# Kernel optimization log

Hardware: AMD Instinct MI355X
Metric: run time of the kernel (lower is better)

Reference implementation:

```python
import jax, jax.numpy as jnp
import numpy as np

N, E = 50000, 800000
IN_F, OUT_F, H = 128, 128, 4
D = OUT_F // H  # head dim
NEG_SLOPE = 0.2
EPS = 1e-12


def setup_inputs() -> dict:
    key = jax.random.key(0)
    ks = jax.random.split(key, 10)
    s = 1.0 / np.sqrt(IN_F)
    return {
        "x": jax.random.normal(ks[0], (N, IN_F), jnp.float32),
        "W_src": jax.random.normal(ks[1], (IN_F, H * D), jnp.float32) * s,
        "b_src": jnp.zeros((H * D,), jnp.float32),
        "W_dst": jax.random.normal(ks[2], (IN_F, H * D), jnp.float32) * s,
        "b_dst": jnp.zeros((H * D,), jnp.float32),
        "attn": jax.random.normal(ks[3], (H, D), jnp.float32) * (1.0 / np.sqrt(D)),
        "out_bias": jnp.zeros((H * D,), jnp.float32),
        "ln_w": jnp.ones((OUT_F,), jnp.float32),
        "ln_b": jnp.zeros((OUT_F,), jnp.float32),
        "src": jax.random.randint(ks[4], (E,), 0, N, jnp.int32),
        "dst": jax.random.randint(ks[5], (E,), 0, N, jnp.int32),
    }


def reference(x, W_src, b_src, W_dst, b_dst, attn, out_bias, ln_w, ln_b, src, dst):
    n = x.shape[0]
    # GATv2Conv (share_weights=False): separate source/dest projections
    fs = (x @ W_src + b_src).reshape(n, H, D)  # [N,H,D]
    fd = (x @ W_dst + b_dst).reshape(n, H, D)
    # per-edge scores: e_ij = attn . leaky_relu(fs[u] + fd[v])
    e = jax.nn.leaky_relu(fs[src] + fd[dst], NEG_SLOPE)  # [E,H,D]
    logits = jnp.einsum("ehd,hd->eh", e, attn)  # [E,H]
    # edge softmax over incoming edges of each dst node
    m = jax.ops.segment_max(logits, dst, num_segments=n)  # [N,H]
    ex = jnp.exp(logits - m[dst])
    denom = jax.ops.segment_sum(ex, dst, num_segments=n)  # [N,H]
    alpha = ex / denom[dst]  # [E,H]
    # aggregate: sum_j alpha_ij * fs[j]
    msg = alpha[:, :, None] * fs[src]  # [E,H,D]
    rst = jax.ops.segment_sum(msg, dst, num_segments=n)  # [N,H,D]
    h = rst.reshape(n, H * D) + out_bias
    # LayerNorm (biased variance, eps inside sqrt)
    u = h.mean(-1, keepdims=True)
    s = jnp.mean((h - u) ** 2, -1, keepdims=True)
    h = (h - u) / jnp.sqrt(s + EPS)
    h = ln_w * h + ln_b
    # activation = elu; dropout p=0 -> identity
    return jax.nn.elu(h)
```

## Files before the change

### kernel.cpp

```cpp
#include <hip/hip_runtime.h>
#include <hip/hip_bf16.h>

constexpr int NF = 128;

using bf16x8 = __attribute__((ext_vector_type(8))) short;
using f32x4v = __attribute__((ext_vector_type(4))) float;

__device__ __forceinline__ unsigned short f2bs(float f) {
    return __builtin_bit_cast(unsigned short, __float2bfloat16(f));
}
__device__ __forceinline__ void unpack8(float4 raw, float* a) {
    unsigned u0 = __float_as_uint(raw.x);
    unsigned u1 = __float_as_uint(raw.y);
    unsigned u2 = __float_as_uint(raw.z);
    unsigned u3 = __float_as_uint(raw.w);
    a[0] = __uint_as_float(u0 << 16);
    a[1] = __uint_as_float(u0 & 0xffff0000u);
    a[2] = __uint_as_float(u1 << 16);
    a[3] = __uint_as_float(u1 & 0xffff0000u);
    a[4] = __uint_as_float(u2 << 16);
    a[5] = __uint_as_float(u2 & 0xffff0000u);
    a[6] = __uint_as_float(u3 << 16);
    a[7] = __uint_as_float(u3 & 0xffff0000u);
}

__global__ void GraphAttnLayer_70196945486348_kernel() {}

__global__ __launch_bounds__(256) void prep_kernel(
    const float* __restrict__ Wsrc, const float* __restrict__ Wdst,
    unsigned short* __restrict__ Wb,
    int* __restrict__ cnt, int* __restrict__ state, int N, int NB)
{
    int i = blockIdx.x * 256 + threadIdx.x;
    if (i < N) cnt[i] = 0;
    if (i < NB) state[i] = 0;
    if (i < 256 * NF) {
        int k   = i >> 8;
        int col = i & 255;
        float v = (col < 128) ? Wsrc[k * NF + col] : Wdst[k * NF + (col - 128)];
        Wb[col * NF + k] = f2bs(v);
    }
}

__global__ __launch_bounds__(256) void gemm_hist_kernel(
    const float* __restrict__ x,
    const unsigned short* __restrict__ Wb,
    const float* __restrict__ bsrc, const float* __restrict__ bdst,
    unsigned short* __restrict__ fs,
    float* __restrict__ fd,
    const int* __restrict__ src, const int* __restrict__ dst,
    int* __restrict__ cnt, int* __restrict__ pack,
    int N, int E, int NGB)
{
    {
        int e = blockIdx.x * 256 + threadIdx.x;
        if (e < E) {
            int r = atomicAdd(&cnt[dst[e]], 1);
            pack[e] = (r << 17) | src[e];
        }
    }
    if (blockIdx.x >= NGB) return;

    const int lane = threadIdx.x & 63;
    const int wave = threadIdx.x >> 6;
    const int m_base = blockIdx.x * 32;
    const int lm = lane & 15;
    const int kq = (lane >> 4) * 8;

    bf16x8 bfrag[4][4];
    float bias[4];
#pragma unroll
    for (int c = 0; c < 4; ++c) {
        int col = wave * 64 + c * 16 + lm;
        bias[c] = (col < 128) ? bsrc[col] : bdst[col - 128];
#pragma unroll
        for (int s = 0; s < 4; ++s)
            bfrag[c][s] = *(const bf16x8*)(Wb + col * NF + s * 32 + kq);
    }

    for (int r = 0; r < 2; ++r) {
        int m0 = m_base + r * 16;
        if (m0 >= N) break;
        int row = m0 + lm;
        if (row >= N) row = N - 1;
        bf16x8 afrag[4];
#pragma unroll
        for (int s = 0; s < 4; ++s) {
            const float4* xp = (const float4*)(x + (size_t)row * NF + s * 32 + kq);
            float4 xa = xp[0], xb = xp[1];
            afrag[s][0] = (short)f2bs(xa.x);
            afrag[s][1] = (short)f2bs(xa.y);
            afrag[s][2] = (short)f2bs(xa.z);
            afrag[s][3] = (short)f2bs(xa.w);
            afrag[s][4] = (short)f2bs(xb.x);
            afrag[s][5] = (short)f2bs(xb.y);
            afrag[s][6] = (short)f2bs(xb.z);
            afrag[s][7] = (short)f2bs(xb.w);
        }
#pragma unroll
        for (int c = 0; c < 4; ++c) {
            f32x4v acc = {0.f, 0.f, 0.f, 0.f};
#pragma unroll
            for (int s = 0; s < 4; ++s)
                acc = __builtin_amdgcn_mfma_f32_16x16x32_bf16(afrag[s], bfrag[c][s], acc, 0, 0, 0);
            int col = wave * 64 + c * 16 + lm;
            int cc = col & 127;
#pragma unroll
            for (int rr = 0; rr < 4; ++rr) {
                int rowd = m0 + (lane >> 4) * 4 + rr;
                if (rowd < N) {
                    float v = acc[rr] + bias[c];
                    if (col < 128) fs[(size_t)rowd * NF + cc] = f2bs(v);
                    else           fd[(size_t)rowd * NF + cc] = v;
                }
            }
        }
    }
}

__global__ __launch_bounds__(256) void scan_kernel(
    const int* __restrict__ cnt, int* __restrict__ rowptr,
    int* __restrict__ state, int N, int E)
{
    int b = blockIdx.x, t = threadIdx.x;
    int i = b * 256 + t;
    int v = (i < N) ? cnt[i] : 0;

    __shared__ int arr[256];
    __shared__ int s_bofs;
    arr[t] = v;
    __syncthreads();
    for (int off = 1; off < 256; off <<= 1) {
        int u = (t >= off) ? arr[t - off] : 0;
        __syncthreads();
        arr[t] += u;
        __syncthreads();
    }
    int total = arr[255];

    if (t < 64) {
        if (t == 0) {
            int word = ((b == 0 ? 2 : 1) << 30) | total;
            atomicExch(&state[b], word);
        }
        int bofs = 0;
        if (b > 0) {
            int base = b;
            for (;;) {
                int j = base - 1 - t;
                int sv = 0, f = 1;
                if (j >= 0) {
                    sv = atomicAdd(&state[j], 0);
                    f = ((unsigned)sv) >> 30;
                }
                unsigned long long notready = __ballot(f == 0);
                if (notready) continue;
                unsigned long long has2 = __ballot(f == 2);
                if (has2) {
                    int k = (int)(__ffsll((unsigned long long)has2) - 1);
                    int val = (t <= k) ? (sv & 0x3FFFFFFF) : 0;
#pragma unroll
                    for (int off = 32; off; off >>= 1) val += __shfl_xor(val, off);
                    bofs += val;
                    break;
                } else {
                    int val = (j >= 0) ? (sv & 0x3FFFFFFF) : 0;
#pragma unroll
                    for (int off = 32; off; off >>= 1) val += __shfl_xor(val, off);
                    bofs += val;
                    base -= 64;
                }
            }
            if (t == 0) atomicExch(&state[b], (2 << 30) | (bofs + total));
        }
        if (t == 0) s_bofs = bofs;
    }
    __syncthreads();
    int bofs = s_bofs;
    int excl = arr[t] - v + bofs;
    if (i < N) rowptr[i] = excl;
    if (i == 0) rowptr[N] = E;
}

__global__ __launch_bounds__(256) void scatter_kernel(
    const int* __restrict__ dst, const int* __restrict__ pack,
    const int* __restrict__ rowptr, int* __restrict__ src_sorted, int E)
{
    int idx = blockIdx.x * 256 + threadIdx.x;
    int e0 = idx * 4;
    if (e0 + 3 < E) {
        int4 d = *(const int4*)(dst + e0);
        int4 p = *(const int4*)(pack + e0);
        src_sorted[rowptr[d.x] + (p.x >> 17)] = p.x & 0x1FFFF;
        src_sorted[rowptr[d.y] + (p.y >> 17)] = p.y & 0x1FFFF;
        src_sorted[rowptr[d.z] + (p.z >> 17)] = p.z & 0x1FFFF;
        src_sorted[rowptr[d.w] + (p.w >> 17)] = p.w & 0x1FFFF;
    } else {
        for (int e = e0; e < E; ++e) {
            int p = pack[e];
            src_sorted[rowptr[dst[e]] + (p >> 17)] = p & 0x1FFFF;
        }
    }
}

__global__ __launch_bounds__(256) void node_kernel(
    const float4* __restrict__ fsq,
    const int* __restrict__ rowptr, const int* __restrict__ src_sorted,
    const float4* __restrict__ attn4,
    const float4* __restrict__ obias4,
    const float4* __restrict__ lnw4,
    const float4* __restrict__ lnb4,
    float4* __restrict__ out4, int N)
{
    int lane = threadIdx.x & 63;
    int es = lane >> 4;
    int g  = lane & 15;
    int n = blockIdx.x * 4 + (threadIdx.x >> 6);
    if (n >= N) return;

    float4 fda = out4[(size_t)n * 32 + g * 2];
    float4 fdb = out4[(size_t)n * 32 + g * 2 + 1];
    float4 ava = attn4[g * 2];
    float4 avb = attn4[g * 2 + 1];
    float fd[8] = {fda.x, fda.y, fda.z, fda.w, fdb.x, fdb.y, fdb.z, fdb.w};
    float av[8] = {ava.x, ava.y, ava.z, ava.w, avb.x, avb.y, avb.z, avb.w};

    int beg = rowptr[n], end = rowptr[n + 1];
    float l = 0.f;
    float ac[8] = {0.f, 0.f, 0.f, 0.f, 0.f, 0.f, 0.f, 0.f};

    for (int j = beg; j < end; j += 4) {
        int idx = j + es;
        bool valid = idx < end;
        int s = src_sorted[valid ? idx : (end - 1)];
        float4 raw = fsq[(size_t)s * 16 + g];
        float a[8];
        unpack8(raw, a);
        float p = 0.f;
#pragma unroll
        for (int d = 0; d < 8; ++d) {
            float t = a[d] + fd[d];
            t = fmaxf(t, 0.2f * t);
            p += av[d] * t;
        }
        p += __shfl_xor(p, 1);
        p += __shfl_xor(p, 2);
        float e = valid ? __expf(p) : 0.f;
        l += e;
#pragma unroll
        for (int d = 0; d < 8; ++d) ac[d] += e * a[d];
    }

    l += __shfl_xor(l, 16);
    l += __shfl_xor(l, 32);
#pragma unroll
    for (int d = 0; d < 8; ++d) {
        ac[d] += __shfl_xor(ac[d], 16);
        ac[d] += __shfl_xor(ac[d], 32);
    }

    float rl = (l > 0.f) ? (1.f / l) : 0.f;
    float4 oba = obias4[g * 2];
    float4 obb = obias4[g * 2 + 1];
    float ob[8] = {oba.x, oba.y, oba.z, oba.w, obb.x, obb.y, obb.z, obb.w};
    float h[8];
    float s1 = 0.f, s2 = 0.f;
#pragma unroll
    for (int d = 0; d < 8; ++d) {
        h[d] = ac[d] * rl + ob[d];
        s1 += h[d];
        s2 += h[d] * h[d];
    }
    s1 += __shfl_xor(s1, 1); s2 += __shfl_xor(s2, 1);
    s1 += __shfl_xor(s1, 2); s2 += __shfl_xor(s2, 2);
    s1 += __shfl_xor(s1, 4); s2 += __shfl_xor(s2, 4);
    s1 += __shfl_xor(s1, 8); s2 += __shfl_xor(s2, 8);

    float u = s1 * (1.f / NF);
    float var = s2 * (1.f / NF) - u * u;
    float rstd = rsqrtf(fmaxf(var, 0.f) + 1e-12f);
    float4 gwa = lnw4[g * 2], gwb = lnw4[g * 2 + 1];
    float4 gba = lnb4[g * 2], gbb = lnb4[g * 2 + 1];
    float gw[8] = {gwa.x, gwa.y, gwa.z, gwa.w, gwb.x, gwb.y, gwb.z, gwb.w};
    float gb[8] = {gba.x, gba.y, gba.z, gba.w, gbb.x, gbb.y, gbb.z, gbb.w};
    float z[8];
#pragma unroll
    for (int d = 0; d < 8; ++d) {
        float y = gw[d] * ((h[d] - u) * rstd) + gb[d];
        z[d] = (y > 0.f) ? y : (__expf(y) - 1.f);
    }
    if (es == 0) {
        out4[(size_t)n * 32 + g * 2]     = make_float4(z[0], z[1], z[2], z[3]);
        out4[(size_t)n * 32 + g * 2 + 1] = make_float4(z[4], z[5], z[6], z[7]);
    }
}

extern "C" void kernel_launch(void* const* d_in, const int* in_sizes, int n_in,
                              void* d_out, int out_size, void* d_ws, size_t ws_size,
                              hipStream_t stream)
{
    const float* x    = (const float*)d_in[0];
    const float* Wsrc = (const float*)d_in[1];
    const float* bsrc = (const float*)d_in[2];
    const float* Wdst = (const float*)d_in[3];
    const float* bdst = (const float*)d_in[4];
    const float4* attn4 = (const float4*)d_in[5];
    const float4* obias4= (const float4*)d_in[6];
    const float4* lnw4  = (const float4*)d_in[7];
    const float4* lnb4  = (const float4*)d_in[8];
    const int* src = (const int*)d_in[9];
    const int* dst = (const int*)d_in[10];
    int N = in_sizes[0] / NF;
    int E = in_sizes[9];
    int NB = (N + 255) / 256;

    int* cnt = (int*)d_ws;
    int* rowptr = cnt + N;
    int* state = rowptr + (N + 1);
    int* pack = state + NB;
    int* srcs = pack + E;
    unsigned short* Wb = (unsigned short*)(srcs + E);
    unsigned short* fs = Wb + 256 * NF;

    int NGB = (N + 31) / 32;
    int GB  = (E + 255) / 256;
    if (GB < NGB) GB = NGB;

    prep_kernel<<<NB, 256, 0, stream>>>(Wsrc, Wdst, Wb, cnt, state, N, NB);
    gemm_hist_kernel<<<GB, 256, 0, stream>>>(
        x, Wb, bsrc, bdst, fs, (float*)d_out, src, dst, cnt, pack, N, E, NGB);
    scan_kernel<<<NB, 256, 0, stream>>>(cnt, rowptr, state, N, E);
    scatter_kernel<<<(E / 4 + 255) / 256, 256, 0, stream>>>(dst, pack, rowptr, srcs, E);
    node_kernel<<<(N + 3) / 4, 256, 0, stream>>>(
        (const float4*)fs, rowptr, srcs, attn4, obias4, lnw4, lnb4,
        (float4*)d_out, N);
}
```

Measured before the change: 212.6 us.

## Move edge histogram into weight-prep kernel and split GEMM into standalone kernel

The edge histogram (atomic counting plus packing) moves from the GEMM kernel into the weight-conversion prep kernel. Zeroing of counts and scan state is replaced by a hipMemsetAsync. The GEMM becomes its own kernel with one 16-row tile per block instead of two, giving more blocks. Smaller changes: the scan's look-back uses a relaxed atomic load instead of atomicAdd(0), the workspace layout puts state next to cnt so one memset covers both, and scatter handles 8 edges per thread. This adds an extra launch (the memset) and serialises histogram and GEMM rather than overlapping them inside one kernel.

```diff
diff --git a/kernel.cpp b/kernel.cpp
--- a/kernel.cpp
+++ b/kernel.cpp
@@ -26,14 +26,19 @@
 
 __global__ void GraphAttnLayer_70196945486348_kernel() {}
 
-__global__ __launch_bounds__(256) void prep_kernel(
+__global__ __launch_bounds__(256) void hist_prep_kernel(
+    const int* __restrict__ src, const int* __restrict__ dst,
+    int* __restrict__ cnt, int* __restrict__ pack,
     const float* __restrict__ Wsrc, const float* __restrict__ Wdst,
     unsigned short* __restrict__ Wb,
-    int* __restrict__ cnt, int* __restrict__ state, int N, int NB)
-{
+    int E)
+{
+    int e = blockIdx.x * 256 + threadIdx.x;
+    if (e < E) {
+        int r = atomicAdd(&cnt[dst[e]], 1);
+        pack[e] = (r << 17) | src[e];
+    }
     int i = blockIdx.x * 256 + threadIdx.x;
-    if (i < N) cnt[i] = 0;
-    if (i < NB) state[i] = 0;
     if (i < 256 * NF) {
         int k   = i >> 8;
         int col = i & 255;
@@ -42,30 +47,20 @@
     }
 }
 
-__global__ __launch_bounds__(256) void gemm_hist_kernel(
+__global__ __launch_bounds__(256) void gemm_kernel(
     const float* __restrict__ x,
     const unsigned short* __restrict__ Wb,
     const float* __restrict__ bsrc, const float* __restrict__ bdst,
     unsigned short* __restrict__ fs,
     float* __restrict__ fd,
-    const int* __restrict__ src, const int* __restrict__ dst,
-    int* __restrict__ cnt, int* __restrict__ pack,
-    int N, int E, int NGB)
-{
-    {
-        int e = blockIdx.x * 256 + threadIdx.x;
-        if (e < E) {
-            int r = atomicAdd(&cnt[dst[e]], 1);
-            pack[e] = (r << 17) | src[e];
-        }
-    }
-    if (blockIdx.x >= NGB) return;
-
+    int N)
+{
     const int lane = threadIdx.x & 63;
     const int wave = threadIdx.x >> 6;
-    const int m_base = blockIdx.x * 32;
+    const int m0 = blockIdx.x * 16;
     const int lm = lane & 15;
     const int kq = (lane >> 4) * 8;
+    if (m0 >= N) return;
 
     bf16x8 bfrag[4][4];
     float bias[4];
@@ -78,41 +73,37 @@
             bfrag[c][s] = *(const bf16x8*)(Wb + col * NF + s * 32 + kq);
     }
 
-    for (int r = 0; r < 2; ++r) {
-        int m0 = m_base + r * 16;
-        if (m0 >= N) break;
-        int row = m0 + lm;
-        if (row >= N) row = N - 1;
-        bf16x8 afrag[4];
-#pragma unroll
-        for (int s = 0; s < 4; ++s) {
-            const float4* xp = (const float4*)(x + (size_t)row * NF + s * 32 + kq);
-            float4 xa = xp[0], xb = xp[1];
-            afrag[s][0] = (short)f2bs(xa.x);
-            afrag[s][1] = (short)f2bs(xa.y);
-            afrag[s][2] = (short)f2bs(xa.z);
-            afrag[s][3] = (short)f2bs(xa.w);
-            afrag[s][4] = (short)f2bs(xb.x);
-            afrag[s][5] = (short)f2bs(xb.y);
-            afrag[s][6] = (short)f2bs(xb.z);
-            afrag[s][7] = (short)f2bs(xb.w);
-        }
-#pragma unroll
-        for (int c = 0; c < 4; ++c) {
-            f32x4v acc = {0.f, 0.f, 0.f, 0.f};
-#pragma unroll
-            for (int s = 0; s < 4; ++s)
-                acc = __builtin_amdgcn_mfma_f32_16x16x32_bf16(afrag[s], bfrag[c][s], acc, 0, 0, 0);
-            int col = wave * 64 + c * 16 + lm;
-            int cc = col & 127;
-#pragma unroll
-            for (int rr = 0; rr < 4; ++rr) {
-                int rowd = m0 + (lane >> 4) * 4 + rr;
-                if (rowd < N) {
-                    float v = acc[rr] + bias[c];
-                    if (col < 128) fs[(size_t)rowd * NF + cc] = f2bs(v);
-                    else           fd[(size_t)rowd * NF + cc] = v;
-                }
+    int row = m0 + lm;
+    if (row >= N) row = N - 1;
+    bf16x8 afrag[4];
+#pragma unroll
+    for (int s = 0; s < 4; ++s) {
+        const float4* xp = (const float4*)(x + (size_t)row * NF + s * 32 + kq);
+        float4 xa = xp[0], xb = xp[1];
+        afrag[s][0] = (short)f2bs(xa.x);
+        afrag[s][1] = (short)f2bs(xa.y);
+        afrag[s][2] = (short)f2bs(xa.z);
+        afrag[s][3] = (short)f2bs(xa.w);
+        afrag[s][4] = (short)f2bs(xb.x);
+        afrag[s][5] = (short)f2bs(xb.y);
+        afrag[s][6] = (short)f2bs(xb.z);
+        afrag[s][7] = (short)f2bs(xb.w);
+    }
+#pragma unroll
+    for (int c = 0; c < 4; ++c) {
+        f32x4v acc = {0.f, 0.f, 0.f, 0.f};
+#pragma unroll
+        for (int s = 0; s < 4; ++s)
+            acc = __builtin_amdgcn_mfma_f32_16x16x32_bf16(afrag[s], bfrag[c][s], acc, 0, 0, 0);
+        int col = wave * 64 + c * 16 + lm;
+        int cc = col & 127;
+#pragma unroll
+        for (int rr = 0; rr < 4; ++rr) {
+            int rowd = m0 + (lane >> 4) * 4 + rr;
+            if (rowd < N) {
+                float v = acc[rr] + bias[c];
+                if (col < 128) fs[(size_t)rowd * NF + cc] = f2bs(v);
+                else           fd[(size_t)rowd * NF + cc] = v;
             }
         }
     }
@@ -150,7 +141,8 @@
                 int j = base - 1 - t;
                 int sv = 0, f = 1;
                 if (j >= 0) {
-                    sv = atomicAdd(&state[j], 0);
+                    sv = __hip_atomic_load(&state[j], __ATOMIC_RELAXED,
+                                           __HIP_MEMORY_SCOPE_AGENT);
                     f = ((unsigned)sv) >> 30;
                 }
                 unsigned long long notready = __ballot(f == 0);
@@ -187,14 +179,20 @@
     const int* __restrict__ rowptr, int* __restrict__ src_sorted, int E)
 {
     int idx = blockIdx.x * 256 + threadIdx.x;
-    int e0 = idx * 4;
-    if (e0 + 3 < E) {
-        int4 d = *(const int4*)(dst + e0);
-        int4 p = *(const int4*)(pack + e0);
-        src_sorted[rowptr[d.x] + (p.x >> 17)] = p.x & 0x1FFFF;
-        src_sorted[rowptr[d.y] + (p.y >> 17)] = p.y & 0x1FFFF;
-        src_sorted[rowptr[d.z] + (p.z >> 17)] = p.z & 0x1FFFF;
-        src_sorted[rowptr[d.w] + (p.w >> 17)] = p.w & 0x1FFFF;
+    int e0 = idx * 8;
+    if (e0 + 7 < E) {
+        int4 d0 = *(const int4*)(dst + e0);
+        int4 d1 = *(const int4*)(dst + e0 + 4);
+        int4 p0 = *(const int4*)(pack + e0);
+        int4 p1 = *(const int4*)(pack + e0 + 4);
+        src_sorted[rowptr[d0.x] + (p0.x >> 17)] = p0.x & 0x1FFFF;
+        src_sorted[rowptr[d0.y] + (p0.y >> 17)] = p0.y & 0x1FFFF;
+        src_sorted[rowptr[d0.z] + (p0.z >> 17)] = p0.z & 0x1FFFF;
+        src_sorted[rowptr[d0.w] + (p0.w >> 17)] = p0.w & 0x1FFFF;
+        src_sorted[rowptr[d1.x] + (p1.x >> 17)] = p1.x & 0x1FFFF;
+        src_sorted[rowptr[d1.y] + (p1.y >> 17)] = p1.y & 0x1FFFF;
+        src_sorted[rowptr[d1.z] + (p1.z >> 17)] = p1.z & 0x1FFFF;
+        src_sorted[rowptr[d1.w] + (p1.w >> 17)] = p1.w & 0x1FFFF;
     } else {
         for (int e = e0; e < E; ++e) {
             int p = pack[e];
@@ -315,22 +313,23 @@
     int NB = (N + 255) / 256;
 
     int* cnt = (int*)d_ws;
-    int* rowptr = cnt + N;
-    int* state = rowptr + (N + 1);
-    int* pack = state + NB;
+    int* state = cnt + N;
+    int* rowptr = state + NB;
+    int* pack = rowptr + (N + 1);
     int* srcs = pack + E;
     unsigned short* Wb = (unsigned short*)(srcs + E);
     unsigned short* fs = Wb + 256 * NF;
 
-    int NGB = (N + 31) / 32;
     int GB  = (E + 255) / 256;
-    if (GB < NGB) GB = NGB;
-
-    prep_kernel<<<NB, 256, 0, stream>>>(Wsrc, Wdst, Wb, cnt, state, N, NB);
-    gemm_hist_kernel<<<GB, 256, 0, stream>>>(
-        x, Wb, bsrc, bdst, fs, (float*)d_out, src, dst, cnt, pack, N, E, NGB);
+    int NGB = (N + 15) / 16;
+
+    hipMemsetAsync(cnt, 0, (size_t)(N + NB) * sizeof(int), stream);
+    hist_prep_kernel<<<GB, 256, 0, stream>>>(src, dst, cnt, pack,
+                                             Wsrc, Wdst, Wb, E);
+    gemm_kernel<<<NGB, 256, 0, stream>>>(x, Wb, bsrc, bdst, fs,
+                                         (float*)d_out, N);
     scan_kernel<<<NB, 256, 0, stream>>>(cnt, rowptr, state, N, E);
-    scatter_kernel<<<(E / 4 + 255) / 256, 256, 0, stream>>>(dst, pack, rowptr, srcs, E);
+    scatter_kernel<<<(E / 8 + 255) / 256, 256, 0, stream>>>(dst, pack, rowptr, srcs, E);
     node_kernel<<<(N + 3) / 4, 256, 0, stream>>>(
         (const float4*)fs, rowptr, srcs, attn4, obias4, lnw4, lnb4,
         (float4*)d_out, N);
```

Result: slower. 237.9 us (+11.9%).

## Privatize degree histogram into eight sub-histograms to cut atomic contention

Applied to the files above, without the earlier changes.

The in-degree histogram is split into eight copies chosen by block index. This is meant to reduce atomic collisions on the same counters and spread the atomics across more cache lines. The scan sums the eight counts per node and writes per-copy start offsets (ptr8), which the scatter kernel then uses to place edges. In exchange, zeroing, the scan's reads and the offset array all grow eightfold, and the scatter does a strided ptr8 lookup. The scan's lookback now uses a relaxed atomic load instead of atomicAdd(0).

```diff
diff --git a/kernel.cpp b/kernel.cpp
--- a/kernel.cpp
+++ b/kernel.cpp
@@ -29,10 +29,10 @@
 __global__ __launch_bounds__(256) void prep_kernel(
     const float* __restrict__ Wsrc, const float* __restrict__ Wdst,
     unsigned short* __restrict__ Wb,
-    int* __restrict__ cnt, int* __restrict__ state, int N, int NB)
+    int* __restrict__ cnt8, int* __restrict__ state, int N8, int NB)
 {
     int i = blockIdx.x * 256 + threadIdx.x;
-    if (i < N) cnt[i] = 0;
+    if (i < N8) cnt8[i] = 0;
     if (i < NB) state[i] = 0;
     if (i < 256 * NF) {
         int k   = i >> 8;
@@ -49,13 +49,14 @@
     unsigned short* __restrict__ fs,
     float* __restrict__ fd,
     const int* __restrict__ src, const int* __restrict__ dst,
-    int* __restrict__ cnt, int* __restrict__ pack,
+    int* __restrict__ cnt8, int* __restrict__ pack,
     int N, int E, int NGB)
 {
     {
         int e = blockIdx.x * 256 + threadIdx.x;
         if (e < E) {
-            int r = atomicAdd(&cnt[dst[e]], 1);
+            int c = blockIdx.x & 7;
+            int r = atomicAdd(&cnt8[c * N + dst[e]], 1);
             pack[e] = (r << 17) | src[e];
         }
     }
@@ -119,16 +120,22 @@
 }
 
 __global__ __launch_bounds__(256) void scan_kernel(
-    const int* __restrict__ cnt, int* __restrict__ rowptr,
-    int* __restrict__ state, int N, int E)
+    const int* __restrict__ cnt8, int* __restrict__ rowptr,
+    int* __restrict__ ptr8, int* __restrict__ state, int N, int E)
 {
     int b = blockIdx.x, t = threadIdx.x;
     int i = b * 256 + t;
-    int v = (i < N) ? cnt[i] : 0;
+
+    int v[8];
+    int tot = 0;
+    if (i < N) {
+#pragma unroll
+        for (int c = 0; c < 8; ++c) { v[c] = cnt8[c * N + i]; tot += v[c]; }
+    }
 
     __shared__ int arr[256];
     __shared__ int s_bofs;
-    arr[t] = v;
+    arr[t] = tot;
     __syncthreads();
     for (int off = 1; off < 256; off <<= 1) {
         int u = (t >= off) ? arr[t - off] : 0;
@@ -150,7 +157,8 @@
                 int j = base - 1 - t;
                 int sv = 0, f = 1;
                 if (j >= 0) {
-                    sv = atomicAdd(&state[j], 0);
+                    sv = __hip_atomic_load(&state[j], __ATOMIC_RELAXED,
+                                           __HIP_MEMORY_SCOPE_AGENT);
                     f = ((unsigned)sv) >> 30;
                 }
                 unsigned long long notready = __ballot(f == 0);
@@ -177,28 +185,38 @@
     }
     __syncthreads();
     int bofs = s_bofs;
-    int excl = arr[t] - v + bofs;
-    if (i < N) rowptr[i] = excl;
+    int excl = arr[t] - tot + bofs;
+    if (i < N) {
+        rowptr[i] = excl;
+        int run = excl;
+#pragma unroll
+        for (int c = 0; c < 8; ++c) { ptr8[i * 8 + c] = run; run += v[c]; }
+    }
     if (i == 0) rowptr[N] = E;
 }
 
 __global__ __launch_bounds__(256) void scatter_kernel(
     const int* __restrict__ dst, const int* __restrict__ pack,
-    const int* __restrict__ rowptr, int* __restrict__ src_sorted, int E)
+    const int* __restrict__ ptr8, int* __restrict__ src_sorted, int E)
 {
     int idx = blockIdx.x * 256 + threadIdx.x;
     int e0 = idx * 4;
     if (e0 + 3 < E) {
         int4 d = *(const int4*)(dst + e0);
         int4 p = *(const int4*)(pack + e0);
-        src_sorted[rowptr[d.x] + (p.x >> 17)] = p.x & 0x1FFFF;
-        src_sorted[rowptr[d.y] + (p.y >> 17)] = p.y & 0x1FFFF;
-        src_sorted[rowptr[d.z] + (p.z >> 17)] = p.z & 0x1FFFF;
-        src_sorted[rowptr[d.w] + (p.w >> 17)] = p.w & 0x1FFFF;
+        int c0 = ((e0 + 0) >> 8) & 7;
+        int c1 = ((e0 + 1) >> 8) & 7;
+        int c2 = ((e0 + 2) >> 8) & 7;
+        int c3 = ((e0 + 3) >> 8) & 7;
+        src_sorted[ptr8[d.x * 8 + c0] + (p.x >> 17)] = p.x & 0x1FFFF;
+        src_sorted[ptr8[d.y * 8 + c1] + (p.y >> 17)] = p.y & 0x1FFFF;
+        src_sorted[ptr8[d.z * 8 + c2] + (p.z >> 17)] = p.z & 0x1FFFF;
+        src_sorted[ptr8[d.w * 8 + c3] + (p.w >> 17)] = p.w & 0x1FFFF;
     } else {
         for (int e = e0; e < E; ++e) {
             int p = pack[e];
-            src_sorted[rowptr[dst[e]] + (p >> 17)] = p & 0x1FFFF;
+            int c = (e >> 8) & 7;
+            src_sorted[ptr8[dst[e] * 8 + c] + (p >> 17)] = p & 0x1FFFF;
         }
     }
 }
@@ -313,11 +331,13 @@
     int N = in_sizes[0] / NF;
     int E = in_sizes[9];
     int NB = (N + 255) / 256;
-
-    int* cnt = (int*)d_ws;
-    int* rowptr = cnt + N;
-    int* state = rowptr + (N + 1);
-    int* pack = state + NB;
+    int N8 = N * 8;
+
+    int* cnt8 = (int*)d_ws;
+    int* state = cnt8 + N8;
+    int* rowptr = state + NB;
+    int* ptr8 = rowptr + (N + 1);
+    int* pack = ptr8 + N8;
     int* srcs = pack + E;
     unsigned short* Wb = (unsigned short*)(srcs + E);
     unsigned short* fs = Wb + 256 * NF;
@@ -325,12 +345,13 @@
     int NGB = (N + 31) / 32;
     int GB  = (E + 255) / 256;
     if (GB < NGB) GB = NGB;
-
-    prep_kernel<<<NB, 256, 0, stream>>>(Wsrc, Wdst, Wb, cnt, state, N, NB);
+    int PB = (N8 + 255) / 256;
+
+    prep_kernel<<<PB, 256, 0, stream>>>(Wsrc, Wdst, Wb, cnt8, state, N8, NB);
     gemm_hist_kernel<<<GB, 256, 0, stream>>>(
-        x, Wb, bsrc, bdst, fs, (float*)d_out, src, dst, cnt, pack, N, E, NGB);
-    scan_kernel<<<NB, 256, 0, stream>>>(cnt, rowptr, state, N, E);
-    scatter_kernel<<<(E / 4 + 255) / 256, 256, 0, stream>>>(dst, pack, rowptr, srcs, E);
+        x, Wb, bsrc, bdst, fs, (float*)d_out, src, dst, cnt8, pack, N, E, NGB);
+    scan_kernel<<<NB, 256, 0, stream>>>(cnt8, rowptr, ptr8, state, N, E);
+    scatter_kernel<<<(E / 4 + 255) / 256, 256, 0, stream>>>(dst, pack, ptr8, srcs, E);
     node_kernel<<<(N + 3) / 4, 256, 0, stream>>>(
         (const float4*)fs, rowptr, srcs, attn4, obias4, lnw4, lnb4,
         (float4*)d_out, N);
```

After: 216.6 us. No clear change (+1.9%).

## Stage GEMM output through LDS, narrow sorted source indices to 16 bits

Applied to the files above, without the earlier changes.

The projection kernel now writes MFMA accumulators into a shared-memory tile and then emits row-contiguous vector stores: 16-byte bf16x8 stores for fs and two float4 stores for fd. This replaces the scattered per-element stores, and costs two extra barriers plus the LDS traffic. Sorted source indices are packed with a 16-bit shift and stored as unsigned short, which halves the index traffic in the scatter and node kernels but limits N to 65536. The decoupled-lookback scan now polls with a relaxed atomic load instead of an atomicAdd of zero.

```diff
diff --git a/kernel.cpp b/kernel.cpp
--- a/kernel.cpp
+++ b/kernel.cpp
@@ -56,11 +56,12 @@
         int e = blockIdx.x * 256 + threadIdx.x;
         if (e < E) {
             int r = atomicAdd(&cnt[dst[e]], 1);
-            pack[e] = (r << 17) | src[e];
+            pack[e] = (r << 16) | src[e];
         }
     }
     if (blockIdx.x >= NGB) return;
 
+    __shared__ float tile[16][258];
     const int lane = threadIdx.x & 63;
     const int wave = threadIdx.x >> 6;
     const int m_base = blockIdx.x * 32;
@@ -104,17 +105,37 @@
             for (int s = 0; s < 4; ++s)
                 acc = __builtin_amdgcn_mfma_f32_16x16x32_bf16(afrag[s], bfrag[c][s], acc, 0, 0, 0);
             int col = wave * 64 + c * 16 + lm;
-            int cc = col & 127;
-#pragma unroll
-            for (int rr = 0; rr < 4; ++rr) {
-                int rowd = m0 + (lane >> 4) * 4 + rr;
-                if (rowd < N) {
-                    float v = acc[rr] + bias[c];
-                    if (col < 128) fs[(size_t)rowd * NF + cc] = f2bs(v);
-                    else           fd[(size_t)rowd * NF + cc] = v;
-                }
+#pragma unroll
+            for (int rr = 0; rr < 4; ++rr)
+                tile[(lane >> 4) * 4 + rr][col] = acc[rr] + bias[c];
+        }
+        __syncthreads();
+        {
+            int t = threadIdx.x;
+            int orow = t >> 4;
+            int ocol = (t & 15) * 8;
+            int grow = m0 + orow;
+            if (grow < N) {
+                bf16x8 v;
+#pragma unroll
+                for (int j = 0; j < 8; ++j)
+                    v[j] = (short)f2bs(tile[orow][ocol + j]);
+                *(bf16x8*)(fs + (size_t)grow * NF + ocol) = v;
+                float4 f0, f1;
+                f0.x = tile[orow][128 + ocol + 0];
+                f0.y = tile[orow][128 + ocol + 1];
+                f0.z = tile[orow][128 + ocol + 2];
+                f0.w = tile[orow][128 + ocol + 3];
+                f1.x = tile[orow][128 + ocol + 4];
+                f1.y = tile[orow][128 + ocol + 5];
+                f1.z = tile[orow][128 + ocol + 6];
+                f1.w = tile[orow][128 + ocol + 7];
+                float4* fp = (float4*)(fd + (size_t)grow * NF + ocol);
+                fp[0] = f0;
+                fp[1] = f1;
             }
         }
+        __syncthreads();
     }
 }
 
@@ -150,7 +171,8 @@
                 int j = base - 1 - t;
                 int sv = 0, f = 1;
                 if (j >= 0) {
-                    sv = atomicAdd(&state[j], 0);
+                    sv = __hip_atomic_load(&state[j], __ATOMIC_RELAXED,
+                                           __HIP_MEMORY_SCOPE_AGENT);
                     f = ((unsigned)sv) >> 30;
                 }
                 unsigned long long notready = __ballot(f == 0);
@@ -184,28 +206,29 @@
 
 __global__ __launch_bounds__(256) void scatter_kernel(
     const int* __restrict__ dst, const int* __restrict__ pack,
-    const int* __restrict__ rowptr, int* __restrict__ src_sorted, int E)
+    const int* __restrict__ rowptr, unsigned short* __restrict__ src_sorted,
+    int E)
 {
     int idx = blockIdx.x * 256 + threadIdx.x;
     int e0 = idx * 4;
     if (e0 + 3 < E) {
         int4 d = *(const int4*)(dst + e0);
         int4 p = *(const int4*)(pack + e0);
-        src_sorted[rowptr[d.x] + (p.x >> 17)] = p.x & 0x1FFFF;
-        src_sorted[rowptr[d.y] + (p.y >> 17)] = p.y & 0x1FFFF;
-        src_sorted[rowptr[d.z] + (p.z >> 17)] = p.z & 0x1FFFF;
-        src_sorted[rowptr[d.w] + (p.w >> 17)] = p.w & 0x1FFFF;
+        src_sorted[rowptr[d.x] + ((unsigned)p.x >> 16)] = (unsigned short)(p.x & 0xFFFF);
+        src_sorted[rowptr[d.y] + ((unsigned)p.y >> 16)] = (unsigned short)(p.y & 0xFFFF);
+        src_sorted[rowptr[d.z] + ((unsigned)p.z >> 16)] = (unsigned short)(p.z & 0xFFFF);
+        src_sorted[rowptr[d.w] + ((unsigned)p.w >> 16)] = (unsigned short)(p.w & 0xFFFF);
     } else {
         for (int e = e0; e < E; ++e) {
             int p = pack[e];
-            src_sorted[rowptr[dst[e]] + (p >> 17)] = p & 0x1FFFF;
+            src_sorted[rowptr[dst[e]] + ((unsigned)p >> 16)] = (unsigned short)(p & 0xFFFF);
         }
     }
 }
 
 __global__ __launch_bounds__(256) void node_kernel(
     const float4* __restrict__ fsq,
-    const int* __restrict__ rowptr, const int* __restrict__ src_sorted,
+    const int* __restrict__ rowptr, const unsigned short* __restrict__ src_sorted,
     const float4* __restrict__ attn4,
     const float4* __restrict__ obias4,
     const float4* __restrict__ lnw4,
@@ -315,11 +338,11 @@
     int NB = (N + 255) / 256;
 
     int* cnt = (int*)d_ws;
-    int* rowptr = cnt + N;
-    int* state = rowptr + (N + 1);
-    int* pack = state + NB;
-    int* srcs = pack + E;
-    unsigned short* Wb = (unsigned short*)(srcs + E);
+    int* state = cnt + N;
+    int* rowptr = state + NB;
+    int* pack = rowptr + (N + 1);
+    unsigned short* srcs = (unsigned short*)(pack + E);
+    unsigned short* Wb = srcs + ((E + 1) & ~1);
     unsigned short* fs = Wb + 256 * NF;
 
     int NGB = (N + 31) / 32;
```

New measurement: 214.2 us. Within noise of the previous version (+0.7%).
